# Kernel optimization log

Hardware: AMD Instinct MI355X
Metric: run time of the kernel (lower is better)

Reference implementation:

```python
import jax, jax.numpy as jnp
import numpy as np
from jax import lax


def _edit_distance(ow, tg):
    # ow: [B, S] int predicted words; tg: [B, T] int targets
    B, S = ow.shape
    T = tg.shape[1]
    f32 = jnp.float32
    row0 = jnp.broadcast_to(jnp.arange(T + 1, dtype=f32), (B, T + 1))  # dp[:,0,:] = j

    def outer(prev_row, oi):  # prev_row: [B, T+1], oi: [B] = output_words[:, i-1]
        mask = (oi[:, None] == tg).astype(f32)          # [B, T]
        up = prev_row[:, 1:]                            # dp[:, i-1, j]
        diag = prev_row[:, :-1]                         # dp[:, i-1, j-1]
        first = prev_row[:, 0] + 1.0                    # dp[:, i, 0] = i

        def inner(left, xs):  # left: [B] = dp[:, i, j-1]
            u, d, m = xs
            new = m * d + (1.0 - m) * (jnp.minimum(jnp.minimum(u, left), d) + 1.0)
            return new, new

        _, rowvals = lax.scan(inner, first, (up.T, diag.T, mask.T))  # [T, B]
        new_row = jnp.concatenate([first[:, None], rowvals.T], axis=1)
        return new_row, None

    final_row, _ = lax.scan(outer, row0, ow.T)  # scan over i = 1..S
    return final_row[:, -1]  # dp[:, S, T]


def setup_inputs() -> dict:
    key = jax.random.key(0)
    k1, k2 = jax.random.split(key)
    output = jax.random.normal(k1, (16, 512, 32000), dtype=jnp.float32)
    target = jax.random.randint(k2, (16, 512), 0, 32000, dtype=jnp.int32)
    return {"output": output, "target": target}


def reference(output, target):
    # softmax does not change argmax but is kept for faithfulness to the original
    probs = jax.nn.softmax(output, axis=-1)
    output_words = jnp.argmax(probs, axis=-1).astype(jnp.int32)  # [B, S]
    dist = _edit_distance(output_words, target)                   # [B]
    T = target.shape[1]
    return jnp.mean(dist / jnp.float32(T))
```

## Files before the change

### kernel.cpp

```cpp
#include <hip/hip_runtime.h>
#include <math.h>

#define VOCAB 32000
#define BATCH 16
#define SEQ   512

__global__ __launch_bounds__(256) void argmax_kernel(const float* __restrict__ logits,
                                                     int* __restrict__ words) {
    const int pos = blockIdx.x;
    const float4* base4 = (const float4*)(logits + (size_t)pos * VOCAB);

    const int tid = threadIdx.x;
    float best = -INFINITY;
    int bestIdx = 0x7FFFFFFF;

    for (int k = tid; k < VOCAB / 4; k += 256) {
        float4 v = base4[k];
        int i0 = k * 4;
        if (v.x > best) { best = v.x; bestIdx = i0;     }
        if (v.y > best) { best = v.y; bestIdx = i0 + 1; }
        if (v.z > best) { best = v.z; bestIdx = i0 + 2; }
        if (v.w > best) { best = v.w; bestIdx = i0 + 3; }
    }

    for (int off = 32; off > 0; off >>= 1) {
        float ov = __shfl_down(best, off, 64);
        int   oi = __shfl_down(bestIdx, off, 64);
        if (ov > best || (ov == best && oi < bestIdx)) { best = ov; bestIdx = oi; }
    }

    __shared__ float sv[4];
    __shared__ int   si[4];
    const int wid = tid >> 6;
    if ((tid & 63) == 0) { sv[wid] = best; si[wid] = bestIdx; }
    __syncthreads();

    if (tid == 0) {
        for (int w = 1; w < 4; ++w) {
            if (sv[w] > best || (sv[w] == best && si[w] < bestIdx)) {
                best = sv[w]; bestIdx = si[w];
            }
        }
        words[pos] = bestIdx;
    }
}

#define RPL 8

__global__ __launch_bounds__(64) void editdist_kernel(const int* __restrict__ words,
                                                      const int* __restrict__ target,
                                                      float* __restrict__ dist) {
    const int b = blockIdx.x;
    const int t = threadIdx.x;

    __shared__ int s_tg[SEQ];
    #pragma unroll
    for (int k = 0; k < RPL; ++k)
        s_tg[t + 64 * k] = target[b * SEQ + t + 64 * k];
    __syncthreads();

    int myw[RPL];
    #pragma unroll
    for (int r = 0; r < RPL; ++r)
        myw[r] = words[b * SEQ + t * RPL + r];

    int colv[RPL];
    #pragma unroll
    for (int r = 0; r < RPL; ++r) colv[r] = t * RPL + 1 + r;
    int prev_up = t * RPL;

    const int NSTEP = SEQ + 64 - 1;
    for (int s = 1; s <= NSTEP; ++s) {
        int up_in = __shfl_up(colv[RPL - 1], 1, 64);
        const int j = s - t;
        if (t == 0) up_in = s;
        if (j >= 1 && j <= SEQ) {
            const int tgj = s_tg[j - 1];
            int u  = up_in;
            int dg = prev_up;
            #pragma unroll
            for (int r = 0; r < RPL; ++r) {
                const int left = colv[r];
                const int de = dg - (myw[r] == tgj ? 1 : 0);
                int mn = u < left ? u : left;
                mn = mn < de ? mn : de;
                const int nc = mn + 1;
                dg = left;
                colv[r] = nc;
                u = nc;
            }
            prev_up = up_in;
        }
    }

    if (t == 63) dist[b] = (float)colv[RPL - 1];
}

__global__ void finalize_kernel(const float* __restrict__ dist, float* __restrict__ out) {
    if (threadIdx.x == 0 && blockIdx.x == 0) {
        float s = 0.0f;
        for (int b = 0; b < BATCH; ++b) s += dist[b];
        out[0] = s / ((float)BATCH * (float)SEQ);
    }
}

extern "C" void kernel_launch(void* const* d_in, const int* in_sizes, int n_in,
                              void* d_out, int out_size, void* d_ws, size_t ws_size,
                              hipStream_t stream) {
    const float* logits = (const float*)d_in[0];
    const int*   target = (const int*)d_in[1];

    int*   words = (int*)d_ws;
    float* dist  = (float*)((char*)d_ws + BATCH * SEQ * sizeof(int));

    argmax_kernel<<<BATCH * SEQ, 256, 0, stream>>>(logits, words);
    editdist_kernel<<<BATCH, 64, 0, stream>>>(words, target, dist);
    finalize_kernel<<<1, 64, 0, stream>>>(dist, (float*)d_out);
}
```

Measured before the change: 270.9 us.

## Use one wavefront per argmax row, restructure DP min chain, drop finalize kernel

The argmax kernel now gives each wavefront a whole row (four rows per block), so the LDS cross-wave reduction and __syncthreads go away. Its logit loads use nontemporal hints and the loop is unrolled. The edit-distance inner loop is split so the diagonal/left minima are computed independently and only a short min(u+1, mp) chain stays serial. The finalize kernel is removed: the output is zeroed in the argmax kernel and accumulated with atomicAdd, which saves a launch but makes the float sum order nondeterministic.

New measurement: 253.3 us (median of 2 runs). 1.07x faster.

```diff
diff --git a/kernel.cpp b/kernel.cpp
--- a/kernel.cpp
+++ b/kernel.cpp
@@ -4,18 +4,26 @@
 #define VOCAB 32000
 #define BATCH 16
 #define SEQ   512
+#define RPL   8
+
+typedef float floatx4 __attribute__((ext_vector_type(4)));
 
 __global__ __launch_bounds__(256) void argmax_kernel(const float* __restrict__ logits,
-                                                     int* __restrict__ words) {
-    const int pos = blockIdx.x;
-    const float4* base4 = (const float4*)(logits + (size_t)pos * VOCAB);
+                                                     int* __restrict__ words,
+                                                     float* __restrict__ out) {
+    if (blockIdx.x == 0 && threadIdx.x == 0) out[0] = 0.0f;
 
-    const int tid = threadIdx.x;
+    const int wid  = threadIdx.x >> 6;
+    const int lane = threadIdx.x & 63;
+    const int row  = blockIdx.x * 4 + wid;
+    const floatx4* base4 = (const floatx4*)(logits + (size_t)row * VOCAB);
+
     float best = -INFINITY;
     int bestIdx = 0x7FFFFFFF;
 
-    for (int k = tid; k < VOCAB / 4; k += 256) {
-        float4 v = base4[k];
+    #pragma unroll 5
+    for (int k = lane; k < VOCAB / 4; k += 64) {
+        floatx4 v = __builtin_nontemporal_load(base4 + k);
         int i0 = k * 4;
         if (v.x > best) { best = v.x; bestIdx = i0;     }
         if (v.y > best) { best = v.y; bestIdx = i0 + 1; }
@@ -28,28 +36,12 @@
         int   oi = __shfl_down(bestIdx, off, 64);
         if (ov > best || (ov == best && oi < bestIdx)) { best = ov; bestIdx = oi; }
     }
-
-    __shared__ float sv[4];
-    __shared__ int   si[4];
-    const int wid = tid >> 6;
-    if ((tid & 63) == 0) { sv[wid] = best; si[wid] = bestIdx; }
-    __syncthreads();
-
-    if (tid == 0) {
-        for (int w = 1; w < 4; ++w) {
-            if (sv[w] > best || (sv[w] == best && si[w] < bestIdx)) {
-                best = sv[w]; bestIdx = si[w];
-            }
-        }
-        words[pos] = bestIdx;
-    }
+    if (lane == 0) words[row] = bestIdx;
 }
-
-#define RPL 8
 
 __global__ __launch_bounds__(64) void editdist_kernel(const int* __restrict__ words,
                                                       const int* __restrict__ target,
-                                                      float* __restrict__ dist) {
+                                                      float* __restrict__ out) {
     const int b = blockIdx.x;
     const int t = threadIdx.x;
 
@@ -69,39 +61,30 @@
     for (int r = 0; r < RPL; ++r) colv[r] = t * RPL + 1 + r;
     int prev_up = t * RPL;
 
-    const int NSTEP = SEQ + 64 - 1;
+    const int NSTEP = SEQ + 63;
     for (int s = 1; s <= NSTEP; ++s) {
         int up_in = __shfl_up(colv[RPL - 1], 1, 64);
         const int j = s - t;
         if (t == 0) up_in = s;
         if (j >= 1 && j <= SEQ) {
             const int tgj = s_tg[j - 1];
-            int u  = up_in;
-            int dg = prev_up;
+            int mp[RPL];
+            mp[0] = min(colv[0], prev_up - (myw[0] == tgj ? 1 : 0)) + 1;
+            #pragma unroll
+            for (int r = 1; r < RPL; ++r)
+                mp[r] = min(colv[r], colv[r - 1] - (myw[r] == tgj ? 1 : 0)) + 1;
+            int u = up_in;
             #pragma unroll
             for (int r = 0; r < RPL; ++r) {
-                const int left = colv[r];
-                const int de = dg - (myw[r] == tgj ? 1 : 0);
-                int mn = u < left ? u : left;
-                mn = mn < de ? mn : de;
-                const int nc = mn + 1;
-                dg = left;
-                colv[r] = nc;
-                u = nc;
+                u = min(u + 1, mp[r]);
+                colv[r] = u;
             }
             prev_up = up_in;
         }
     }
 
-    if (t == 63) dist[b] = (float)colv[RPL - 1];
-}
-
-__global__ void finalize_kernel(const float* __restrict__ dist, float* __restrict__ out) {
-    if (threadIdx.x == 0 && blockIdx.x == 0) {
-        float s = 0.0f;
-        for (int b = 0; b < BATCH; ++b) s += dist[b];
-        out[0] = s / ((float)BATCH * (float)SEQ);
-    }
+    if (t == 63)
+        atomicAdd(out, (float)colv[RPL - 1] * (1.0f / ((float)BATCH * (float)SEQ)));
 }
 
 extern "C" void kernel_launch(void* const* d_in, const int* in_sizes, int n_in,
@@ -110,10 +93,9 @@
     const float* logits = (const float*)d_in[0];
     const int*   target = (const int*)d_in[1];
 
-    int*   words = (int*)d_ws;
-    float* dist  = (float*)((char*)d_ws + BATCH * SEQ * sizeof(int));
+    int* words = (int*)d_ws;
+    float* out = (float*)d_out;
 
-    argmax_kernel<<<BATCH * SEQ, 256, 0, stream>>>(logits, words);
-    editdist_kernel<<<BATCH, 64, 0, stream>>>(words, target, dist);
-    finalize_kernel<<<1, 64, 0, stream>>>(dist, (float*)d_out);
+    argmax_kernel<<<BATCH * SEQ / 4, 256, 0, stream>>>(logits, words, out);
+    editdist_kernel<<<BATCH, 64, 0, stream>>>(words, target, out);
 }
```
